# Kernel tuning notes

Hardware: AMD Instinct MI355X
Metric: run time of the kernel (lower is better)

Reference implementation:

```python
import jax, jax.numpy as jnp
import numpy as np

H = 70  # hidden size == input size


def _renorm_rows(w, max_norm=1.0, eps=1e-7):
    # emulate nn.Embedding(max_norm=1.0): clip row L2 norm to <= 1
    n = jnp.linalg.norm(w, axis=-1, keepdims=True)
    return jnp.where(n > max_norm, w * (max_norm / (n + eps)), w)


def _lstm(x, w_ih, w_hh, b_ih, b_hh):
    # x: (B, T, H). PyTorch gate order: i, f, g, o.
    B = x.shape[0]
    xg = jnp.einsum('bth,gh->btg', x, w_ih) + (b_ih + b_hh)  # (B, T, 4H)
    def step(carry, xt):
        h, c = carry
        gates = xt + h @ w_hh.T  # (B, 4H)
        i, f, g, o = jnp.split(gates, 4, axis=-1)
        i = jax.nn.sigmoid(i); f = jax.nn.sigmoid(f)
        g = jnp.tanh(g); o = jax.nn.sigmoid(o)
        c = f * c + i * g
        h = o * jnp.tanh(c)
        return (h, c), h
    h0 = jnp.zeros((B, H), x.dtype)
    (_, _), hs = jax.lax.scan(step, (h0, h0), jnp.swapaxes(xg, 0, 1))
    return jnp.swapaxes(hs, 0, 1)  # (B, T, H)


def setup_inputs() -> dict:
    key = jax.random.key(0)
    ks = jax.random.split(key, 12)
    B, S, C = 128, 512, 1104
    s = 0.1
    return {
        'x': jax.random.uniform(ks[0], (B, S, C), jnp.float32),
        'embed_w': jax.random.normal(ks[1], (C, H), jnp.float32),
        'w_ih': jax.random.normal(ks[2], (4 * H, H), jnp.float32) * s,
        'w_hh': jax.random.normal(ks[3], (4 * H, H), jnp.float32) * s,
        'b_ih': jax.random.normal(ks[4], (4 * H,), jnp.float32) * s,
        'b_hh': jax.random.normal(ks[5], (4 * H,), jnp.float32) * s,
        'attn_w1': jax.random.normal(ks[6], (64, H), jnp.float32) * s,
        'attn_b1': jax.random.normal(ks[7], (64,), jnp.float32) * s,
        'attn_w2': jax.random.normal(ks[8], (1, 64), jnp.float32) * s,
        'attn_b2': jax.random.normal(ks[9], (1,), jnp.float32) * s,
        'fc_w': jax.random.normal(ks[10], (3, H), jnp.float32) * s,
        'fc_b': jax.random.normal(ks[11], (3,), jnp.float32) * s,
    }


def reference(x, embed_w, w_ih, w_hh, b_ih, b_hh, attn_w1, attn_b1, attn_w2, attn_b2, fc_w, fc_b):
    w = _renorm_rows(embed_w)                      # (C, H)
    # fused form of (x[...,None] * weight).sum(dim=2): plain GEMM
    e = jnp.einsum('bsc,ch->bsh', x, w)            # (B, S, H)
    out = _lstm(e, w_ih, w_hh, b_ih, b_hh)         # (B, S, H)
    # self-attention pooling
    energy = jax.nn.relu(out @ attn_w1.T + attn_b1) @ attn_w2.T + attn_b2  # (B,S,1)
    weights = jax.nn.softmax(energy[..., 0], axis=1)                        # (B,S)
    pooled = jnp.einsum('bsh,bs->bh', out, weights)                         # (B,H)
    # dropout is identity at eval
    logits = pooled @ fc_w.T + fc_b
    return jax.nn.softmax(logits, axis=1)
```

## Files before the change

kernel.cpp:

```cpp
#include <hip/hip_runtime.h>
#include <math.h>

#define HDIM 70
#define HPAD 72
#define GATES 280
#define NG 288
#define TLEN 512
#define BATCH 128
#define CDIM 1104
#define KW 1152
#define ROWS 65536

#define OFF_WRN   0
#define OFF_BIAS  77312
#define OFF_WCT   77632
#define OFF_XG    243520
#define OFF_HOUT  9418560
#define OFF_EN    14137152

typedef short short8 __attribute__((ext_vector_type(8)));
typedef float f32x4 __attribute__((ext_vector_type(4)));

__device__ __forceinline__ unsigned short f2bf(float f) {
    unsigned int u = __float_as_uint(f);
    u = (u + 0x7fffu + ((u >> 16) & 1u)) >> 16;
    return (unsigned short)u;
}
__device__ __forceinline__ float bf2f(unsigned short s) {
    return __uint_as_float(((unsigned int)s) << 16);
}

__global__ __launch_bounds__(64) void k_renorm(const float* __restrict__ w,
                                               float* __restrict__ wrn) {
    const int row = blockIdx.x;
    const int lane = threadIdx.x;
    const float* wr = w + row * HDIM;
    float v0 = wr[lane];
    float v1 = (lane < 6) ? wr[64 + lane] : 0.0f;
    float ss = v0 * v0 + v1 * v1;
    #pragma unroll
    for (int off = 32; off > 0; off >>= 1) ss += __shfl_down(ss, off);
    float tot = __shfl(ss, 0);
    float n = sqrtf(tot);
    float scale = (n > 1.0f) ? 1.0f / (n + 1e-7f) : 1.0f;
    wrn[row * HDIM + lane] = v0 * scale;
    if (lane < 6) wrn[row * HDIM + 64 + lane] = v1 * scale;
}

__global__ __launch_bounds__(256) void k_prep(const float* __restrict__ wrn,
                                              const float* __restrict__ w_ih,
                                              const float* __restrict__ b_ih,
                                              const float* __restrict__ b_hh,
                                              unsigned short* __restrict__ wcT,
                                              float* __restrict__ bias) {
    const int n = blockIdx.x;
    const int tid = threadIdx.x;
    float wr[HDIM];
    if (n < GATES) {
        #pragma unroll
        for (int h = 0; h < HDIM; ++h) wr[h] = w_ih[n * HDIM + h];
        if (tid == 0) bias[n] = b_ih[n] + b_hh[n];
    } else {
        #pragma unroll
        for (int h = 0; h < HDIM; ++h) wr[h] = 0.0f;
    }
    for (int c = tid; c < KW; c += 256) {
        float a = 0.0f;
        if (n < GATES && c < CDIM) {
            const float* wc = wrn + c * HDIM;
            #pragma unroll
            for (int h = 0; h < HDIM; ++h) a += wr[h] * wc[h];
        }
        wcT[(size_t)n * KW + c] = f2bf(a);
    }
}

__global__ __launch_bounds__(256, 2) void k_xg_gemm(const float* __restrict__ x,
                                                    const unsigned short* __restrict__ wcT,
                                                    const float* __restrict__ bias,
                                                    unsigned short* __restrict__ xg) {
    __shared__ __align__(16) unsigned short A_lds[128 * 72];
    __shared__ __align__(16) unsigned short B_lds[NG * 72];
    const int tid = threadIdx.x;
    const int lane = tid & 63;
    const int w = tid >> 6;
    const int mh = (w >> 1) * 64;
    const int nh = (w & 1) * 144;
    const int l15 = lane & 15;
    const int q = lane >> 4;
    const size_t rbase = (size_t)blockIdx.x * 128;

    f32x4 acc[4][9];
    #pragma unroll
    for (int mt = 0; mt < 4; ++mt)
        #pragma unroll
        for (int nt = 0; nt < 9; ++nt) acc[mt][nt] = (f32x4){0.f, 0.f, 0.f, 0.f};

    const int r_st = tid >> 1;
    const int kh_st = (tid & 1) * 32;

    for (int kc = 0; kc < 18; ++kc) {
        const int k0 = kc * 64;
        {
            const float* xr = x + (rbase + r_st) * (size_t)CDIM + k0 + kh_st;
            unsigned short* dst = &A_lds[r_st * 72 + kh_st];
            #pragma unroll
            for (int qq = 0; qq < 8; ++qq) {
                const int kk = k0 + kh_st + qq * 4;
                float4 v = make_float4(0.f, 0.f, 0.f, 0.f);
                if (kk < CDIM) v = *(const float4*)(xr + qq * 4);
                unsigned int lo = (unsigned int)f2bf(v.x) | ((unsigned int)f2bf(v.y) << 16);
                unsigned int hi = (unsigned int)f2bf(v.z) | ((unsigned int)f2bf(v.w) << 16);
                uint2 pv; pv.x = lo; pv.y = hi;
                *(uint2*)&dst[qq * 4] = pv;
            }
        }
        {
            #pragma unroll
            for (int p = 0; p < 9; ++p) {
                const int cid = tid + p * 256;
                const int n = cid >> 3;
                const int ko = (cid & 7) * 8;
                uint4 v = *(const uint4*)(wcT + (size_t)n * KW + k0 + ko);
                *(uint4*)&B_lds[n * 72 + ko] = v;
            }
        }
        __syncthreads();
        #pragma unroll
        for (int ks = 0; ks < 2; ++ks) {
            short8 a[4];
            short8 bfr[9];
            #pragma unroll
            for (int mt = 0; mt < 4; ++mt)
                a[mt] = *(const short8*)&A_lds[(mh + mt * 16 + l15) * 72 + ks * 32 + q * 8];
            #pragma unroll
            for (int nt = 0; nt < 9; ++nt)
                bfr[nt] = *(const short8*)&B_lds[(nh + nt * 16 + l15) * 72 + ks * 32 + q * 8];
            #pragma unroll
            for (int mt = 0; mt < 4; ++mt)
                #pragma unroll
                for (int nt = 0; nt < 9; ++nt)
                    acc[mt][nt] = __builtin_amdgcn_mfma_f32_16x16x32_bf16(a[mt], bfr[nt], acc[mt][nt], 0, 0, 0);
        }
        __syncthreads();
    }
    #pragma unroll
    for (int nt = 0; nt < 9; ++nt) {
        const int n_g = nh + nt * 16 + l15;
        if (n_g >= GATES) continue;
        const float bv = bias[n_g];
        #pragma unroll
        for (int mt = 0; mt < 4; ++mt) {
            #pragma unroll
            for (int r = 0; r < 4; ++r) {
                const size_t row = rbase + mh + mt * 16 + q * 4 + r;
                xg[row * GATES + n_g] = f2bf(acc[mt][nt][r] + bv);
            }
        }
    }
}

__device__ __forceinline__ float tanh_fast(float v) {
    v = fminf(fmaxf(v, -20.0f), 20.0f);
    float E = __expf(2.0f * v);
    return (E - 1.0f) / (E + 1.0f);
}
__device__ __forceinline__ float sigmoid_fast(float v) {
    return 1.0f / (1.0f + __expf(-v));
}

#define PF 8
__global__ __launch_bounds__(320) void k_lstm(const unsigned short* __restrict__ xg,
                                              const float* __restrict__ w_hh,
                                              float* __restrict__ hout) {
    __shared__ __align__(16) float h_lds[HPAD];
    __shared__ float gates_lds[GATES];
    const int tid = threadIdx.x;
    const int b = blockIdx.x;
    float whh[HPAD];
    if (tid < GATES) {
        #pragma unroll
        for (int j = 0; j < HDIM; ++j) whh[j] = w_hh[tid * HDIM + j];
        whh[70] = whh[71] = 0.0f;
    } else {
        #pragma unroll
        for (int j = 0; j < HPAD; ++j) whh[j] = 0.0f;
    }
    if (tid < HPAD) h_lds[tid] = 0.0f;
    float c_reg = 0.0f;

    const unsigned short* xp = xg + (size_t)b * TLEN * GATES + (tid < GATES ? tid : 0);
    float xbuf[PF];
    #pragma unroll
    for (int i = 0; i < PF; ++i) xbuf[i] = bf2f(xp[i * GATES]);
    __syncthreads();

    #pragma unroll 8
    for (int t = 0; t < TLEN; ++t) {
        const int slot = t & (PF - 1);
        const float xcur = xbuf[slot];
        xbuf[slot] = bf2f(xp[((t + PF) & (TLEN - 1)) * GATES]);
        float a0 = 0.f, a1 = 0.f, a2 = 0.f, a3 = 0.f;
        #pragma unroll
        for (int jj = 0; jj < 18; ++jj) {
            float4 hv = ((const float4*)h_lds)[jj];
            a0 += hv.x * whh[4 * jj];
            a1 += hv.y * whh[4 * jj + 1];
            a2 += hv.z * whh[4 * jj + 2];
            a3 += hv.w * whh[4 * jj + 3];
        }
        const float acc = xcur + ((a0 + a1) + (a2 + a3));
        if (tid < GATES) {
            float a;
            if (tid < 140)      a = sigmoid_fast(acc);
            else if (tid < 210) a = tanh_fast(acc);
            else                a = sigmoid_fast(acc);
            gates_lds[tid] = a;
        }
        __syncthreads();
        if (tid < HDIM) {
            const float iv = gates_lds[tid];
            const float fv = gates_lds[tid + 70];
            const float gv = gates_lds[tid + 140];
            const float ov = gates_lds[tid + 210];
            c_reg = fv * c_reg + iv * gv;
            const float hn = ov * tanh_fast(c_reg);
            h_lds[tid] = hn;
            hout[((size_t)b * TLEN + t) * HPAD + tid] = hn;
        }
        __syncthreads();
    }
}

__global__ __launch_bounds__(256) void k_energy(const float* __restrict__ hout,
                                                const float* __restrict__ w1,
                                                const float* __restrict__ b1,
                                                const float* __restrict__ w2,
                                                const float* __restrict__ b2,
                                                float* __restrict__ energy) {
    const int lane = threadIdx.x & 63;
    const int wid = blockIdx.x * 4 + (threadIdx.x >> 6);
    float w1r[HPAD];
    #pragma unroll
    for (int c = 0; c < HDIM; ++c) w1r[c] = w1[lane * HDIM + c];
    w1r[70] = w1r[71] = 0.0f;
    const float b1v = b1[lane];
    const float w2v = w2[lane];
    const float b2v = b2[0];
    for (int row = wid; row < ROWS; row += 4096) {
        const float4* rp = (const float4*)(hout + (size_t)row * HPAD);
        float a0 = 0.f, a1 = 0.f, a2 = 0.f, a3 = 0.f;
        #pragma unroll
        for (int jj = 0; jj < 18; ++jj) {
            float4 v = rp[jj];
            a0 += v.x * w1r[4 * jj];
            a1 += v.y * w1r[4 * jj + 1];
            a2 += v.z * w1r[4 * jj + 2];
            a3 += v.w * w1r[4 * jj + 3];
        }
        float hid = fmaxf((a0 + a1) + (a2 + a3) + b1v, 0.0f) * w2v;
        #pragma unroll
        for (int off = 32; off > 0; off >>= 1) hid += __shfl_down(hid, off);
        if (lane == 0) energy[row] = hid + b2v;
    }
}

__global__ __launch_bounds__(128) void k_pool(const float* __restrict__ hout,
                                              const float* __restrict__ energy,
                                              const float* __restrict__ fc_w,
                                              const float* __restrict__ fc_b,
                                              float* __restrict__ outp) {
    __shared__ float red[128];
    __shared__ float wexp[TLEN];
    __shared__ float pooledL[HDIM];
    const int tid = threadIdx.x;
    const int b = blockIdx.x;
    float v[4];
    #pragma unroll
    for (int k = 0; k < 4; ++k) v[k] = energy[b * TLEN + tid + 128 * k];
    float m = fmaxf(fmaxf(v[0], v[1]), fmaxf(v[2], v[3]));
    red[tid] = m; __syncthreads();
    for (int s = 64; s > 0; s >>= 1) {
        if (tid < s) red[tid] = fmaxf(red[tid], red[tid + s]);
        __syncthreads();
    }
    const float M = red[0]; __syncthreads();
    float s4 = 0.f;
    #pragma unroll
    for (int k = 0; k < 4; ++k) {
        float ex = __expf(v[k] - M);
        wexp[tid + 128 * k] = ex;
        s4 += ex;
    }
    red[tid] = s4; __syncthreads();
    for (int s = 64; s > 0; s >>= 1) {
        if (tid < s) red[tid] += red[tid + s];
        __syncthreads();
    }
    const float rinv = 1.0f / red[0];
    if (tid < HDIM) {
        float a0 = 0.f, a1 = 0.f, a2 = 0.f, a3 = 0.f;
        const float* hp = hout + (size_t)b * TLEN * HPAD + tid;
        for (int s = 0; s < TLEN; s += 4) {
            a0 += wexp[s]     * hp[(size_t)(s)     * HPAD];
            a1 += wexp[s + 1] * hp[(size_t)(s + 1) * HPAD];
            a2 += wexp[s + 2] * hp[(size_t)(s + 2) * HPAD];
            a3 += wexp[s + 3] * hp[(size_t)(s + 3) * HPAD];
        }
        pooledL[tid] = ((a0 + a1) + (a2 + a3)) * rinv;
    }
    __syncthreads();
    if (tid == 0) {
        float l[3];
        #pragma unroll
        for (int i = 0; i < 3; ++i) {
            float a = fc_b[i];
            for (int h = 0; h < HDIM; ++h) a += fc_w[i * HDIM + h] * pooledL[h];
            l[i] = a;
        }
        float m3 = fmaxf(l[0], fmaxf(l[1], l[2]));
        float e0 = __expf(l[0] - m3), e1 = __expf(l[1] - m3), e2 = __expf(l[2] - m3);
        float rs = 1.0f / (e0 + e1 + e2);
        outp[b * 3 + 0] = e0 * rs;
        outp[b * 3 + 1] = e1 * rs;
        outp[b * 3 + 2] = e2 * rs;
    }
}

extern "C" void kernel_launch(void* const* d_in, const int* in_sizes, int n_in,
                              void* d_out, int out_size, void* d_ws, size_t ws_size,
                              hipStream_t stream) {
    const float* x       = (const float*)d_in[0];
    const float* embed_w = (const float*)d_in[1];
    const float* w_ih    = (const float*)d_in[2];
    const float* w_hh    = (const float*)d_in[3];
    const float* b_ih    = (const float*)d_in[4];
    const float* b_hh    = (const float*)d_in[5];
    const float* aw1     = (const float*)d_in[6];
    const float* ab1     = (const float*)d_in[7];
    const float* aw2     = (const float*)d_in[8];
    const float* ab2     = (const float*)d_in[9];
    const float* fc_w    = (const float*)d_in[10];
    const float* fc_b    = (const float*)d_in[11];
    float* outp = (float*)d_out;
    float* ws = (float*)d_ws;

    float* wrn  = ws + OFF_WRN;
    float* bias = ws + OFF_BIAS;
    unsigned short* wcT = (unsigned short*)(ws + OFF_WCT);
    unsigned short* xgp = (unsigned short*)(ws + OFF_XG);
    float* ho = ws + OFF_HOUT;
    float* en = ws + OFF_EN;

    k_renorm<<<CDIM, 64, 0, stream>>>(embed_w, wrn);
    k_prep<<<NG, 256, 0, stream>>>(wrn, w_ih, b_ih, b_hh, wcT, bias);
    k_xg_gemm<<<512, 256, 0, stream>>>(x, wcT, bias, xgp);
    k_lstm<<<BATCH, 320, 0, stream>>>(xgp, w_hh, ho);
    k_energy<<<1024, 256, 0, stream>>>(ho, aw1, ab1, aw2, ab2, en);
    k_pool<<<BATCH, 128, 0, stream>>>(ho, en, fc_w, fc_b, outp);
}
```

Measured before the change: 861.9 us.

## Restructure LSTM step: per-unit gate ownership, split-K shuffles, double-buffered h

The recurrent LSTM kernel now assigns each hidden unit to 16-lane groups across 5 waves. Each lane holds a 20-wide K slice of all four gate rows, and partial dot products are reduced with cross-lane xor shuffles. The owning lane then computes all four gates plus the cell update directly, which removes the gate LDS staging and one of the two block barriers per timestep by double-buffering h. This shortens the serial per-step critical path, at the cost of more registers per thread and gate/x prefetch work concentrated on a quarter of the lanes.

```diff
diff --git a/kernel.cpp b/kernel.cpp
--- a/kernel.cpp
+++ b/kernel.cpp
@@ -170,65 +170,95 @@
 }
 
 #define PF 8
+#define KCH 20
+#define HP2 80
+
 __global__ __launch_bounds__(320) void k_lstm(const unsigned short* __restrict__ xg,
                                               const float* __restrict__ w_hh,
                                               float* __restrict__ hout) {
-    __shared__ __align__(16) float h_lds[HPAD];
-    __shared__ float gates_lds[GATES];
+    __shared__ __align__(16) float h_lds[2][HP2];
     const int tid = threadIdx.x;
     const int b = blockIdx.x;
-    float whh[HPAD];
-    if (tid < GATES) {
-        #pragma unroll
-        for (int j = 0; j < HDIM; ++j) whh[j] = w_hh[tid * HDIM + j];
-        whh[70] = whh[71] = 0.0f;
-    } else {
-        #pragma unroll
-        for (int j = 0; j < HPAD; ++j) whh[j] = 0.0f;
-    }
-    if (tid < HPAD) h_lds[tid] = 0.0f;
+    const int wv = tid >> 6;
+    const int l = tid & 63;
+    const int jj = l & 15;
+    const int kq = l >> 4;
+    const int j = wv * 16 + jj;
+    const bool jvalid = (j < HDIM);
+    const bool lead = (kq == 0) && jvalid;
+
+    float wr0[KCH], wr1[KCH], wr2[KCH], wr3[KCH];
+    #pragma unroll
+    for (int kk = 0; kk < KCH; ++kk) {
+        const int k = kq * KCH + kk;
+        const bool kv = jvalid && (k < HDIM);
+        wr0[kk] = kv ? w_hh[(0 * HDIM + j) * HDIM + k] : 0.0f;
+        wr1[kk] = kv ? w_hh[(1 * HDIM + j) * HDIM + k] : 0.0f;
+        wr2[kk] = kv ? w_hh[(2 * HDIM + j) * HDIM + k] : 0.0f;
+        wr3[kk] = kv ? w_hh[(3 * HDIM + j) * HDIM + k] : 0.0f;
+    }
+
+    if (tid < 2 * HP2) ((float*)h_lds)[tid] = 0.0f;
     float c_reg = 0.0f;
 
-    const unsigned short* xp = xg + (size_t)b * TLEN * GATES + (tid < GATES ? tid : 0);
-    float xbuf[PF];
-    #pragma unroll
-    for (int i = 0; i < PF; ++i) xbuf[i] = bf2f(xp[i * GATES]);
+    const unsigned short* xp = xg + (size_t)b * TLEN * GATES;
+    float xb0[PF], xb1[PF], xb2[PF], xb3[PF];
+    if (lead) {
+        #pragma unroll
+        for (int i = 0; i < PF; ++i) {
+            xb0[i] = bf2f(xp[i * GATES + 0 * HDIM + j]);
+            xb1[i] = bf2f(xp[i * GATES + 1 * HDIM + j]);
+            xb2[i] = bf2f(xp[i * GATES + 2 * HDIM + j]);
+            xb3[i] = bf2f(xp[i * GATES + 3 * HDIM + j]);
+        }
+    }
     __syncthreads();
 
+    int cur = 0;
     #pragma unroll 8
     for (int t = 0; t < TLEN; ++t) {
         const int slot = t & (PF - 1);
-        const float xcur = xbuf[slot];
-        xbuf[slot] = bf2f(xp[((t + PF) & (TLEN - 1)) * GATES]);
+        f32x4 hv[5];
+        const f32x4* hp4 = (const f32x4*)&h_lds[cur][kq * KCH];
+        #pragma unroll
+        for (int qi = 0; qi < 5; ++qi) hv[qi] = hp4[qi];
+
         float a0 = 0.f, a1 = 0.f, a2 = 0.f, a3 = 0.f;
         #pragma unroll
-        for (int jj = 0; jj < 18; ++jj) {
-            float4 hv = ((const float4*)h_lds)[jj];
-            a0 += hv.x * whh[4 * jj];
-            a1 += hv.y * whh[4 * jj + 1];
-            a2 += hv.z * whh[4 * jj + 2];
-            a3 += hv.w * whh[4 * jj + 3];
-        }
-        const float acc = xcur + ((a0 + a1) + (a2 + a3));
-        if (tid < GATES) {
-            float a;
-            if (tid < 140)      a = sigmoid_fast(acc);
-            else if (tid < 210) a = tanh_fast(acc);
-            else                a = sigmoid_fast(acc);
-            gates_lds[tid] = a;
-        }
-        __syncthreads();
-        if (tid < HDIM) {
-            const float iv = gates_lds[tid];
-            const float fv = gates_lds[tid + 70];
-            const float gv = gates_lds[tid + 140];
-            const float ov = gates_lds[tid + 210];
+        for (int qi = 0; qi < 5; ++qi) {
+            #pragma unroll
+            for (int e = 0; e < 4; ++e) {
+                const float hvv = hv[qi][e];
+                const int kk = qi * 4 + e;
+                a0 = fmaf(hvv, wr0[kk], a0);
+                a1 = fmaf(hvv, wr1[kk], a1);
+                a2 = fmaf(hvv, wr2[kk], a2);
+                a3 = fmaf(hvv, wr3[kk], a3);
+            }
+        }
+        a0 += __shfl_xor(a0, 16); a1 += __shfl_xor(a1, 16);
+        a2 += __shfl_xor(a2, 16); a3 += __shfl_xor(a3, 16);
+        a0 += __shfl_xor(a0, 32); a1 += __shfl_xor(a1, 32);
+        a2 += __shfl_xor(a2, 32); a3 += __shfl_xor(a3, 32);
+
+        if (lead) {
+            const float xi = xb0[slot], xf = xb1[slot], xg_ = xb2[slot], xo = xb3[slot];
+            const int tp = (t + PF) & (TLEN - 1);
+            xb0[slot] = bf2f(xp[tp * GATES + 0 * HDIM + j]);
+            xb1[slot] = bf2f(xp[tp * GATES + 1 * HDIM + j]);
+            xb2[slot] = bf2f(xp[tp * GATES + 2 * HDIM + j]);
+            xb3[slot] = bf2f(xp[tp * GATES + 3 * HDIM + j]);
+            const float iv = sigmoid_fast(a0 + xi);
+            const float fv = sigmoid_fast(a1 + xf);
+            const float gv = tanh_fast(a2 + xg_);
+            const float ov = sigmoid_fast(a3 + xo);
             c_reg = fv * c_reg + iv * gv;
             const float hn = ov * tanh_fast(c_reg);
-            h_lds[tid] = hn;
-            hout[((size_t)b * TLEN + t) * HPAD + tid] = hn;
-        }
-        __syncthreads();
+            h_lds[cur ^ 1][j] = hn;
+            hout[((size_t)b * TLEN + t) * HPAD + j] = hn;
+        }
+        __syncthreads();
+        cur ^= 1;
     }
 }
 
```

After: 974.6 us. 13.1% more time.

## Interleave LSTM gates across lanes and exchange via DPP to drop a barrier

Applied to the files above, without the earlier changes.

Each group of four lanes now handles the i, f, g, o gates for one hidden unit. The gate activations are broadcast within that quad with DPP quad_perm moves instead of going through shared memory. A double-buffered h array lets each timestep use a single __syncthreads instead of two. This shortens the serial per-step latency of the recurrence, at the cost of every thread in the quad redundantly computing the cell update and a tanh.

```diff
diff --git a/kernel.cpp b/kernel.cpp
--- a/kernel.cpp
+++ b/kernel.cpp
@@ -173,62 +173,70 @@
 __global__ __launch_bounds__(320) void k_lstm(const unsigned short* __restrict__ xg,
                                               const float* __restrict__ w_hh,
                                               float* __restrict__ hout) {
-    __shared__ __align__(16) float h_lds[HPAD];
-    __shared__ float gates_lds[GATES];
+    __shared__ __align__(16) float h_lds[2][HPAD];
     const int tid = threadIdx.x;
     const int b = blockIdx.x;
+    const int w = tid >> 6;
+    const int l = tid & 63;
+    const int jm = l >> 2;
+    const int g = l & 3;
+    const int j = w * 16 + jm;
+    const bool jv = (j < HDIM);
+
     float whh[HPAD];
-    if (tid < GATES) {
-        #pragma unroll
-        for (int j = 0; j < HDIM; ++j) whh[j] = w_hh[tid * HDIM + j];
+    if (jv) {
+        const float* wr = w_hh + (size_t)(g * HDIM + j) * HDIM;
+        #pragma unroll
+        for (int k = 0; k < HDIM; ++k) whh[k] = wr[k];
         whh[70] = whh[71] = 0.0f;
     } else {
         #pragma unroll
-        for (int j = 0; j < HPAD; ++j) whh[j] = 0.0f;
-    }
-    if (tid < HPAD) h_lds[tid] = 0.0f;
+        for (int k = 0; k < HPAD; ++k) whh[k] = 0.0f;
+    }
+    if (tid < 2 * HPAD) ((float*)h_lds)[tid] = 0.0f;
     float c_reg = 0.0f;
 
-    const unsigned short* xp = xg + (size_t)b * TLEN * GATES + (tid < GATES ? tid : 0);
+    const int goff = jv ? (g * HDIM + j) : 0;
+    const unsigned short* xp = xg + (size_t)b * TLEN * GATES + goff;
     float xbuf[PF];
     #pragma unroll
     for (int i = 0; i < PF; ++i) xbuf[i] = bf2f(xp[i * GATES]);
     __syncthreads();
 
+    int cur = 0;
     #pragma unroll 8
     for (int t = 0; t < TLEN; ++t) {
         const int slot = t & (PF - 1);
         const float xcur = xbuf[slot];
         xbuf[slot] = bf2f(xp[((t + PF) & (TLEN - 1)) * GATES]);
+
+        const f32x4* hp4 = (const f32x4*)h_lds[cur];
         float a0 = 0.f, a1 = 0.f, a2 = 0.f, a3 = 0.f;
         #pragma unroll
-        for (int jj = 0; jj < 18; ++jj) {
-            float4 hv = ((const float4*)h_lds)[jj];
-            a0 += hv.x * whh[4 * jj];
-            a1 += hv.y * whh[4 * jj + 1];
-            a2 += hv.z * whh[4 * jj + 2];
-            a3 += hv.w * whh[4 * jj + 3];
+        for (int kk = 0; kk < 18; ++kk) {
+            f32x4 hv = hp4[kk];
+            a0 = fmaf(hv.x, whh[4 * kk + 0], a0);
+            a1 = fmaf(hv.y, whh[4 * kk + 1], a1);
+            a2 = fmaf(hv.z, whh[4 * kk + 2], a2);
+            a3 = fmaf(hv.w, whh[4 * kk + 3], a3);
         }
         const float acc = xcur + ((a0 + a1) + (a2 + a3));
-        if (tid < GATES) {
-            float a;
-            if (tid < 140)      a = sigmoid_fast(acc);
-            else if (tid < 210) a = tanh_fast(acc);
-            else                a = sigmoid_fast(acc);
-            gates_lds[tid] = a;
-        }
-        __syncthreads();
-        if (tid < HDIM) {
-            const float iv = gates_lds[tid];
-            const float fv = gates_lds[tid + 70];
-            const float gv = gates_lds[tid + 140];
-            const float ov = gates_lds[tid + 210];
-            c_reg = fv * c_reg + iv * gv;
-            const float hn = ov * tanh_fast(c_reg);
-            h_lds[tid] = hn;
-            hout[((size_t)b * TLEN + t) * HPAD + tid] = hn;
-        }
-        __syncthreads();
+        const float act = (g == 2) ? tanh_fast(acc) : sigmoid_fast(acc);
+
+        const int ai = __float_as_int(act);
+        const float i_v = __int_as_float(__builtin_amdgcn_mov_dpp(ai, 0x00, 0xF, 0xF, true));
+        const float f_v = __int_as_float(__builtin_amdgcn_mov_dpp(ai, 0x55, 0xF, 0xF, true));
+        const float t_v = __int_as_float(__builtin_amdgcn_mov_dpp(ai, 0xAA, 0xF, 0xF, true));
+        const float o_v = __int_as_float(__builtin_amdgcn_mov_dpp(ai, 0xFF, 0xF, 0xF, true));
+
+        c_reg = f_v * c_reg + i_v * t_v;
+        const float hn = o_v * tanh_fast(c_reg);
+        if (g == 0 && jv) {
+            h_lds[cur ^ 1][j] = hn;
+            hout[((size_t)b * TLEN + t) * HPAD + j] = hn;
+        }
+        __syncthreads();
+        cur ^= 1;
     }
 }
 
```

After: 841.6 us. 2.3% less time.

## Restructure LSTM step: per-hidden thread pairs, DPP gate exchange, one barrier

Applied to the files above, without the earlier changes.

The recurrent kernel now assigns two lanes to each hidden unit. Each lane computes half of the K-reduction for all four gates, and the two halves are combined with DPP swaps. The gate activations are then exchanged across the lane pair with DPP instead of going through a shared-memory gates array. A double-buffered h array lets each timestep use a single barrier instead of two, and tanh is rewritten in terms of sigmoid. Block size drops from 320 to 192, and each thread holds 144 weights in registers, which raises register pressure.

```diff
diff --git a/kernel.cpp b/kernel.cpp
--- a/kernel.cpp
+++ b/kernel.cpp
@@ -160,75 +160,99 @@
     }
 }
 
-__device__ __forceinline__ float tanh_fast(float v) {
-    v = fminf(fmaxf(v, -20.0f), 20.0f);
-    float E = __expf(2.0f * v);
-    return (E - 1.0f) / (E + 1.0f);
-}
 __device__ __forceinline__ float sigmoid_fast(float v) {
     return 1.0f / (1.0f + __expf(-v));
 }
 
+#define DPPF(x, ctrl) __int_as_float(__builtin_amdgcn_mov_dpp(__float_as_int(x), (ctrl), 0xF, 0xF, true))
+
 #define PF 8
-__global__ __launch_bounds__(320) void k_lstm(const unsigned short* __restrict__ xg,
+__global__ __launch_bounds__(192) void k_lstm(const unsigned short* __restrict__ xg,
                                               const float* __restrict__ w_hh,
                                               float* __restrict__ hout) {
-    __shared__ __align__(16) float h_lds[HPAD];
-    __shared__ float gates_lds[GATES];
+    __shared__ __align__(16) float h_lds[2][HPAD];
     const int tid = threadIdx.x;
     const int b = blockIdx.x;
-    float whh[HPAD];
-    if (tid < GATES) {
-        #pragma unroll
-        for (int j = 0; j < HDIM; ++j) whh[j] = w_hh[tid * HDIM + j];
-        whh[70] = whh[71] = 0.0f;
-    } else {
-        #pragma unroll
-        for (int j = 0; j < HPAD; ++j) whh[j] = 0.0f;
-    }
-    if (tid < HPAD) h_lds[tid] = 0.0f;
+    const int jl = tid >> 1;
+    const int kh = tid & 1;
+    const bool jv = (jl < HDIM);
+
+    const float s0 = kh ? 2.0f : 1.0f;
+    const float m0 = kh ? 2.0f : 1.0f;
+    const float c0 = kh ? -1.0f : 0.0f;
+
+    float wr0[36], wr1[36], wr2[36], wr3[36];
+    #pragma unroll
+    for (int kk = 0; kk < 36; ++kk) {
+        const int k = kh * 36 + kk;
+        const bool kv = jv && (k < HDIM);
+        const size_t base = (size_t)jl * HDIM + k;
+        wr0[kk] = kv ? w_hh[base] : 0.0f;
+        wr1[kk] = kv ? w_hh[1 * HDIM * HDIM + base] : 0.0f;
+        wr2[kk] = kv ? w_hh[2 * HDIM * HDIM + base] : 0.0f;
+        wr3[kk] = kv ? w_hh[3 * HDIM * HDIM + base] : 0.0f;
+    }
+    if (tid < 2 * HPAD) ((float*)h_lds)[tid] = 0.0f;
     float c_reg = 0.0f;
 
-    const unsigned short* xp = xg + (size_t)b * TLEN * GATES + (tid < GATES ? tid : 0);
-    float xbuf[PF];
-    #pragma unroll
-    for (int i = 0; i < PF; ++i) xbuf[i] = bf2f(xp[i * GATES]);
+    const int jc = jv ? jl : 0;
+    const unsigned short* xpA = xg + (size_t)b * TLEN * GATES + kh * 140 + jc;
+    const unsigned short* xpB = xpA + 70;
+    float xbA[PF], xbB[PF];
+    #pragma unroll
+    for (int i = 0; i < PF; ++i) {
+        xbA[i] = bf2f(xpA[i * GATES]);
+        xbB[i] = bf2f(xpB[i * GATES]);
+    }
     __syncthreads();
 
     #pragma unroll 8
     for (int t = 0; t < TLEN; ++t) {
         const int slot = t & (PF - 1);
-        const float xcur = xbuf[slot];
-        xbuf[slot] = bf2f(xp[((t + PF) & (TLEN - 1)) * GATES]);
+        const int cu = t & 1;
+        const float uA = xbA[slot];
+        const float uB = xbB[slot];
+        const int tp = (t + PF) & (TLEN - 1);
+        xbA[slot] = bf2f(xpA[tp * GATES]);
+        xbB[slot] = bf2f(xpB[tp * GATES]);
+
+        const f32x4* hp4 = (const f32x4*)&h_lds[cu][kh * 36];
         float a0 = 0.f, a1 = 0.f, a2 = 0.f, a3 = 0.f;
         #pragma unroll
-        for (int jj = 0; jj < 18; ++jj) {
-            float4 hv = ((const float4*)h_lds)[jj];
-            a0 += hv.x * whh[4 * jj];
-            a1 += hv.y * whh[4 * jj + 1];
-            a2 += hv.z * whh[4 * jj + 2];
-            a3 += hv.w * whh[4 * jj + 3];
-        }
-        const float acc = xcur + ((a0 + a1) + (a2 + a3));
-        if (tid < GATES) {
-            float a;
-            if (tid < 140)      a = sigmoid_fast(acc);
-            else if (tid < 210) a = tanh_fast(acc);
-            else                a = sigmoid_fast(acc);
-            gates_lds[tid] = a;
-        }
-        __syncthreads();
-        if (tid < HDIM) {
-            const float iv = gates_lds[tid];
-            const float fv = gates_lds[tid + 70];
-            const float gv = gates_lds[tid + 140];
-            const float ov = gates_lds[tid + 210];
-            c_reg = fv * c_reg + iv * gv;
-            const float hn = ov * tanh_fast(c_reg);
-            h_lds[tid] = hn;
-            hout[((size_t)b * TLEN + t) * HPAD + tid] = hn;
-        }
-        __syncthreads();
+        for (int qi = 0; qi < 9; ++qi) {
+            f32x4 hv = hp4[qi];
+            #pragma unroll
+            for (int e = 0; e < 4; ++e) {
+                const float hvv = hv[e];
+                const int kk = qi * 4 + e;
+                a0 = fmaf(hvv, wr0[kk], a0);
+                a1 = fmaf(hvv, wr1[kk], a1);
+                a2 = fmaf(hvv, wr2[kk], a2);
+                a3 = fmaf(hvv, wr3[kk], a3);
+            }
+        }
+        a0 += DPPF(a0, 0xB1); a1 += DPPF(a1, 0xB1);
+        a2 += DPPF(a2, 0xB1); a3 += DPPF(a3, 0xB1);
+
+        const float t0 = (kh ? a2 : a0) + uA;
+        const float t1 = (kh ? a3 : a1) + uB;
+        const float act0 = fmaf(m0, sigmoid_fast(s0 * t0), c0);
+        const float act1 = sigmoid_fast(t1);
+
+        const float i_v = DPPF(act0, 0xA0);
+        const float f_v = DPPF(act1, 0xA0);
+        const float g_v = DPPF(act0, 0xF5);
+        const float o_v = DPPF(act1, 0xF5);
+
+        c_reg = fmaf(f_v, c_reg, i_v * g_v);
+        const float hn = o_v * fmaf(2.0f, sigmoid_fast(2.0f * c_reg), -1.0f);
+        if (kh == 0 && jv) {
+            h_lds[cu ^ 1][jl] = hn;
+            hout[((size_t)b * TLEN + t) * HPAD + jl] = hn;
+        }
+        asm volatile("s_waitcnt lgkmcnt(0)" ::: "memory");
+        __builtin_amdgcn_s_barrier();
+        __builtin_amdgcn_sched_barrier(0);
     }
 }
 
@@ -355,7 +379,7 @@
     k_renorm<<<CDIM, 64, 0, stream>>>(embed_w, wrn);
     k_prep<<<NG, 256, 0, stream>>>(wrn, w_ih, b_ih, b_hh, wcT, bias);
     k_xg_gemm<<<512, 256, 0, stream>>>(x, wcT, bias, xgp);
-    k_lstm<<<BATCH, 320, 0, stream>>>(xgp, w_hh, ho);
+    k_lstm<<<BATCH, 192, 0, stream>>>(xgp, w_hh, ho);
     k_energy<<<1024, 256, 0, stream>>>(ho, aw1, ab1, aw2, ab2, en);
     k_pool<<<BATCH, 128, 0, stream>>>(ho, en, fc_w, fc_b, outp);
 }
```

Result: faster. 824.3 us (-4.4%).
